# Kernel optimization log

Measured on AMD Instinct MI355X. Metric: run time of the kernel, lower is better.

Reference implementation:

```python
import jax, jax.numpy as jnp
import numpy as np

N_NODES = 100000
N_EDGES = 3200000
IN_F, HID, OUT = 24, 64, 1


def _gcn_conv(x, W, b, src, dst, norm, n):
    # x: [N, Fin] -> h: [N, Fout]; PyG GCNConv: lin first, then normalized aggregation, then bias
    h = x @ W                                    # [N, Fout]
    msg = h[src] * norm[:, None]                 # [E+N, Fout] gathered, norm-weighted messages
    agg = jax.ops.segment_sum(msg, dst, num_segments=n)  # scatter-add to targets
    return agg + b


def setup_inputs() -> dict:
    key = jax.random.key(0)
    k1, k2, k3, k4 = jax.random.split(key, 4)
    x = jax.random.normal(k1, (N_NODES, IN_F), dtype=jnp.float32)
    edge_index = jax.random.randint(k2, (2, N_EDGES), 0, N_NODES, dtype=jnp.int64)
    # Glorot-ish init for weights
    W1 = jax.random.normal(k3, (IN_F, HID), dtype=jnp.float32) / np.sqrt(IN_F)
    b1 = jnp.zeros((HID,), dtype=jnp.float32)
    W2 = jax.random.normal(k4, (HID, OUT), dtype=jnp.float32) / np.sqrt(HID)
    b2 = jnp.zeros((OUT,), dtype=jnp.float32)
    return {"x": x, "edge_index": edge_index, "W1": W1, "b1": b1, "W2": W2, "b2": b2}


def reference(x, edge_index, W1, b1, W2, b2):
    n = x.shape[0]
    # add self-loops (PyG GCNConv default)
    loops = jnp.arange(n, dtype=edge_index.dtype)
    src = jnp.concatenate([edge_index[0], loops])
    dst = jnp.concatenate([edge_index[1], loops])
    # symmetric normalization: deg over targets of A+I, norm_e = d^-1/2[src] * d^-1/2[dst]
    deg = jax.ops.segment_sum(jnp.ones_like(dst, dtype=x.dtype), dst, num_segments=n)
    dinv = jnp.where(deg > 0, jax.lax.rsqrt(deg), 0.0)
    norm = dinv[src] * dinv[dst]
    h = _gcn_conv(x, W1, b1, src, dst, norm, n)
    h = jax.nn.relu(h)
    # F.dropout with training=self.training -> identity in eval mode (reference runs eval)
    out = _gcn_conv(h, W2, b2, src, dst, norm, n)
    return out
```

## Files before the change

### kernel.cpp

```cpp
#include <hip/hip_runtime.h>
#include <hip/hip_fp16.h>

#define IN_F 24
#define HID 64
#define NB 512
#define NPB 256
#define GSZ_MAX 256
#define PBUF 7168
#define SRC_BITS 17

typedef unsigned int u32;

__device__ __forceinline__ int bucket_lo(int b, int n) {
    return (int)(((long long)b * n + NB - 1) / NB);
}

__global__ __launch_bounds__(256) void k_pcount(const int* __restrict__ dst,
                                                u32* __restrict__ pc, int e, int n) {
    __shared__ u32 h[NB];
    for (int j = threadIdx.x; j < NB; j += 256) h[j] = 0;
    __syncthreads();
    int blk = blockIdx.x;
    long long begin = (long long)e * blk / NPB;
    long long end   = (long long)e * (blk + 1) / NPB;
    for (long long i = begin + threadIdx.x; i < end; i += 256) {
        int k = (int)((long long)dst[i] * NB / n);
        atomicAdd(&h[k], 1u);
    }
    __syncthreads();
    for (int j = threadIdx.x; j < NB; j += 256) pc[(size_t)blk * NB + j] = h[j];
}

__global__ __launch_bounds__(256) void k_pscan_a(u32* __restrict__ pc,
                                                 u32* __restrict__ colsum) {
    __shared__ u32 ps[256];
    int t = blockIdx.x;
    int tid = threadIdx.x;
    u32 v = pc[(size_t)tid * NB + t];
    ps[tid] = v;
    __syncthreads();
    for (int off = 1; off < 256; off <<= 1) {
        u32 v2 = (tid >= off) ? ps[tid - off] : 0;
        __syncthreads();
        ps[tid] += v2;
        __syncthreads();
    }
    pc[(size_t)tid * NB + t] = ps[tid] - v;
    if (tid == 255) colsum[t] = ps[255];
}

__global__ void k_pscan_b(const u32* __restrict__ colsum, u32* __restrict__ basep) {
    __shared__ u32 s[NB];
    int t = threadIdx.x;
    u32 v = colsum[t];
    s[t] = v;
    __syncthreads();
    for (int off = 1; off < NB; off <<= 1) {
        u32 v2 = (t >= off) ? s[t - off] : 0;
        __syncthreads();
        s[t] += v2;
        __syncthreads();
    }
    basep[t] = s[t] - v;
}

__global__ __launch_bounds__(256) void k_part(const int* __restrict__ src,
                                              const int* __restrict__ dst,
                                              const u32* __restrict__ pc,
                                              const u32* __restrict__ basep,
                                              u32* __restrict__ pairs, int e, int n) {
    __shared__ u32 cur[NB];
    int blk = (blockIdx.x & 7) * (NPB / 8) + (blockIdx.x >> 3);
    for (int j = threadIdx.x; j < NB; j += 256)
        cur[j] = pc[(size_t)blk * NB + j] + basep[j];
    __syncthreads();
    long long begin = (long long)e * blk / NPB;
    long long end   = (long long)e * (blk + 1) / NPB;
    for (long long i = begin + threadIdx.x; i < end; i += 256) {
        int d = dst[i];
        int sv = src[i];
        int k = (int)((long long)d * NB / n);
        u32 loc = (u32)(d - bucket_lo(k, n));
        u32 pos = atomicAdd(&cur[k], 1u);
        pairs[pos] = (loc << SRC_BITS) | (u32)sv;
    }
}

__global__ __launch_bounds__(256) void k_bucket(const u32* __restrict__ pairs,
                                                const u32* __restrict__ basep,
                                                const float* __restrict__ x,
                                                int* __restrict__ cnt,
                                                int* __restrict__ row_start,
                                                float* __restrict__ dinv,
                                                int* __restrict__ csr_src,
                                                __half2* __restrict__ xs2, int e, int n) {
    __shared__ u32 pbuf[PBUF];
    __shared__ u32 h[GSZ_MAX];
    __shared__ u32 cur[GSZ_MAX];
    __shared__ u32 sc[GSZ_MAX];
    __shared__ float dloc[GSZ_MAX];
    int b = blockIdx.x;
    int lo = bucket_lo(b, n);
    int hi = bucket_lo(b + 1, n);
    int gsz = hi - lo;
    u32 start = basep[b];
    u32 endp = (b + 1 < NB) ? basep[b + 1] : (u32)e;
    int nbp = (int)(endp - start);
    for (int j = threadIdx.x; j < GSZ_MAX; j += 256) h[j] = 0;
    __syncthreads();
    int stored = nbp < PBUF ? nbp : PBUF;
    for (int i = threadIdx.x; i < stored; i += 256) {
        u32 p = pairs[start + i];
        pbuf[i] = p;
        atomicAdd(&h[p >> SRC_BITS], 1u);
    }
    for (int i = PBUF + threadIdx.x; i < nbp; i += 256) {
        atomicAdd(&h[pairs[start + i] >> SRC_BITS], 1u);
    }
    __syncthreads();
    int t = threadIdx.x;
    u32 v = h[t];
    sc[t] = v;
    __syncthreads();
    for (int off = 1; off < 256; off <<= 1) {
        u32 v2 = (t >= off) ? sc[t - off] : 0;
        __syncthreads();
        sc[t] += v2;
        __syncthreads();
    }
    u32 excl = sc[t] - v;
    if (t < gsz) {
        float dv = rsqrtf((float)(v + 1));
        cnt[lo + t] = (int)v;
        row_start[lo + t] = (int)(start + excl);
        dinv[lo + t] = dv;
        dloc[t] = dv;
        cur[t] = excl;
    }
    __syncthreads();
    for (int i = threadIdx.x; i < stored; i += 256) {
        u32 p = pbuf[i];
        u32 pos = atomicAdd(&cur[p >> SRC_BITS], 1u);
        csr_src[start + pos] = (int)(p & ((1u << SRC_BITS) - 1));
    }
    for (int i = PBUF + threadIdx.x; i < nbp; i += 256) {
        u32 p = pairs[start + i];
        u32 pos = atomicAdd(&cur[p >> SRC_BITS], 1u);
        csr_src[start + pos] = (int)(p & ((1u << SRC_BITS) - 1));
    }
    const float2* xf = (const float2*)(x + (long long)lo * IN_F);
    for (int i = threadIdx.x; i < gsz * 12; i += 256) {
        float2 vv = xf[i];
        float dn = dloc[i / 12];
        xs2[(long long)lo * 12 + i] = __floats2half2_rn(vv.x * dn, vv.y * dn);
    }
}

__global__ __launch_bounds__(256) void k_agg_hz(const float* __restrict__ x,
                                                const __half2* __restrict__ xs2,
                                                const float* __restrict__ dinv,
                                                const int* __restrict__ row_start,
                                                const int* __restrict__ cnt,
                                                const int* __restrict__ csr_src,
                                                const float* __restrict__ W1,
                                                const float* __restrict__ b1,
                                                const float* __restrict__ W2,
                                                float* __restrict__ zs, int n) {
    __shared__ float w[IN_F * HID];
    __shared__ float w2s[HID];
    __shared__ float b1s[HID];
    for (int j = threadIdx.x; j < IN_F * HID; j += 256) w[j] = W1[j];
    if (threadIdx.x < HID) { w2s[threadIdx.x] = W2[threadIdx.x]; b1s[threadIdx.x] = b1[threadIdx.x]; }
    __syncthreads();
    int g = threadIdx.x >> 3;
    int f4 = threadIdx.x & 7;
    int node = blockIdx.x * 32 + g;
    if (node >= n) return;
    float dn = dinv[node];
    const uint2* xq = (const uint2*)xs2;
    float ax0 = 0.0f, ay0 = 0.0f, ax1 = 0.0f, ay1 = 0.0f;
    if (f4 < 6) {
        int row = row_start[node];
        int c = cnt[node];
        float a0 = 0.0f, b0 = 0.0f, c0 = 0.0f, d0 = 0.0f;
        float a1 = 0.0f, b1v = 0.0f, c1 = 0.0f, d1 = 0.0f;
        int j = 0;
        for (; j + 16 <= c; j += 16) {
            const int* cp = csr_src + row + j;
            int s[16];
#pragma unroll
            for (int t = 0; t < 16; ++t) s[t] = cp[t];
            uint2 u[16];
#pragma unroll
            for (int t = 0; t < 16; ++t) u[t] = xq[(size_t)((u32)s[t] * 6u + (u32)f4)];
#pragma unroll
            for (int t = 0; t < 16; t += 2) {
                float2 e0 = __half22float2(__builtin_bit_cast(__half2, u[t].x));
                float2 e1 = __half22float2(__builtin_bit_cast(__half2, u[t].y));
                float2 o0 = __half22float2(__builtin_bit_cast(__half2, u[t + 1].x));
                float2 o1 = __half22float2(__builtin_bit_cast(__half2, u[t + 1].y));
                a0 += e0.x; b0 += e0.y; c0 += e1.x; d0 += e1.y;
                a1 += o0.x; b1v += o0.y; c1 += o1.x; d1 += o1.y;
            }
        }
        for (; j + 8 <= c; j += 8) {
            const int* cp = csr_src + row + j;
            int s[8];
#pragma unroll
            for (int t = 0; t < 8; ++t) s[t] = cp[t];
            uint2 u[8];
#pragma unroll
            for (int t = 0; t < 8; ++t) u[t] = xq[(size_t)((u32)s[t] * 6u + (u32)f4)];
#pragma unroll
            for (int t = 0; t < 8; t += 2) {
                float2 e0 = __half22float2(__builtin_bit_cast(__half2, u[t].x));
                float2 e1 = __half22float2(__builtin_bit_cast(__half2, u[t].y));
                float2 o0 = __half22float2(__builtin_bit_cast(__half2, u[t + 1].x));
                float2 o1 = __half22float2(__builtin_bit_cast(__half2, u[t + 1].y));
                a0 += e0.x; b0 += e0.y; c0 += e1.x; d0 += e1.y;
                a1 += o0.x; b1v += o0.y; c1 += o1.x; d1 += o1.y;
            }
        }
        for (; j < c; ++j) {
            int s = csr_src[row + j];
            uint2 u = xq[(size_t)((u32)s * 6u + (u32)f4)];
            float2 e0 = __half22float2(__builtin_bit_cast(__half2, u.x));
            float2 e1 = __half22float2(__builtin_bit_cast(__half2, u.y));
            a0 += e0.x; b0 += e0.y; c0 += e1.x; d0 += e1.y;
        }
        ax0 = a0 + a1; ay0 = b0 + b1v; ax1 = c0 + c1; ay1 = d0 + d1;
        float4 sx4 = *(const float4*)(x + (long long)node * IN_F + 4 * f4);
        ax0 = (ax0 + sx4.x * dn) * dn;
        ay0 = (ay0 + sx4.y * dn) * dn;
        ax1 = (ax1 + sx4.z * dn) * dn;
        ay1 = (ay1 + sx4.w * dn) * dn;
    }
    int fb = f4 * 8;
    float h[8];
#pragma unroll
    for (int jj = 0; jj < 8; ++jj) h[jj] = b1s[fb + jj];
#pragma unroll
    for (int k = 0; k < IN_F; ++k) {
        int sl = k >> 2;
        int r = k & 3;
        float xv;
        if (r == 0)      xv = __shfl(ax0, sl, 8);
        else if (r == 1) xv = __shfl(ay0, sl, 8);
        else if (r == 2) xv = __shfl(ax1, sl, 8);
        else             xv = __shfl(ay1, sl, 8);
        const float* wr = w + k * HID + fb;
#pragma unroll
        for (int jj = 0; jj < 8; ++jj) h[jj] += xv * wr[jj];
    }
    float p = 0.0f;
#pragma unroll
    for (int jj = 0; jj < 8; ++jj) p += fmaxf(h[jj], 0.0f) * w2s[fb + jj];
    p += __shfl_down(p, 4, 8);
    p += __shfl_down(p, 2, 8);
    p += __shfl_down(p, 1, 8);
    if (f4 == 0) zs[node] = p * dn;
}

__global__ void k_out(const float* __restrict__ zs, const float* __restrict__ dinv,
                      const int* __restrict__ row_start, const int* __restrict__ cnt,
                      const int* __restrict__ csr_src, const float* __restrict__ b2,
                      float* __restrict__ out, int n) {
    int t = blockIdx.x * blockDim.x + threadIdx.x;
    int node = t >> 4;
    int lane = t & 15;
    if (node >= n) return;
    int row = row_start[node];
    int c = cnt[node];
    float v = 0.0f;
    for (int j = lane; j < c; j += 16) {
        v += zs[csr_src[row + j]];
    }
    v += __shfl_down(v, 8, 16);
    v += __shfl_down(v, 4, 16);
    v += __shfl_down(v, 2, 16);
    v += __shfl_down(v, 1, 16);
    if (lane == 0) {
        out[node] = b2[0] + dinv[node] * (zs[node] + v);
    }
}

extern "C" void kernel_launch(void* const* d_in, const int* in_sizes, int n_in,
                              void* d_out, int out_size, void* d_ws, size_t ws_size,
                              hipStream_t stream) {
    const float* x   = (const float*)d_in[0];
    const int*   ei  = (const int*)d_in[1];
    const float* W1  = (const float*)d_in[2];
    const float* b1  = (const float*)d_in[3];
    const float* W2  = (const float*)d_in[4];
    const float* b2  = (const float*)d_in[5];
    float* out = (float*)d_out;

    const int n = in_sizes[0] / IN_F;
    const int e = in_sizes[1] / 2;
    const int* src = ei;
    const int* dst = ei + e;

    const int B = 256;

    char* base = (char*)d_ws;
    u32* pairs     = (u32*)base;
    float* zs      = (float*)base;
    size_t ov = ((size_t)e * 4 + 255) & ~(size_t)255;
    char* after    = base + ov;
    int* cnt       = (int*)after;
    int* row_start = cnt + n;
    int* csr_src   = row_start + n;
    float* dinv    = (float*)(csr_src + e);
    __half* xs     = (__half*)(dinv + n);
    u32* pc        = (u32*)(xs + (size_t)n * IN_F);
    u32* colsum    = pc + (size_t)NPB * NB;
    u32* basep     = colsum + NB;

    k_pcount<<<NPB, B, 0, stream>>>(dst, pc, e, n);
    k_pscan_a<<<NB, B, 0, stream>>>(pc, colsum);
    k_pscan_b<<<1, NB, 0, stream>>>(colsum, basep);
    k_part<<<NPB, B, 0, stream>>>(src, dst, pc, basep, pairs, e, n);
    k_bucket<<<NB, B, 0, stream>>>(pairs, basep, x, cnt, row_start, dinv, csr_src,
                                   (__half2*)xs, e, n);

    k_agg_hz<<<(n + 31) / 32, B, 0, stream>>>(x, (const __half2*)xs, dinv,
                                              row_start, cnt, csr_src,
                                              W1, b1, W2, zs, n);

    const long long n16 = (long long)n * 16;
    k_out<<<(int)((n16 + B - 1) / B), B, 0, stream>>>(zs, dinv, row_start, cnt, csr_src, b2, out, n);
}
```

Before: 218.1 us.

## Split feature gather into two half-width passes over separate fp16 tables

The fp16 scaled-feature table is stored as two separate 12-feature halves, and the layer-1 aggregation now runs as two kernels. Each kernel gathers only one half, so the random-access working set per pass is halved (2.4MB instead of 4.8MB) and more of it can stay in cache. The first pass writes partial aggregates to a workspace buffer, and the second reads them back before applying W1, ReLU and W2. The cost is a second traversal of the CSR indices, an extra intermediate write and read, and one more kernel launch.

```diff
diff --git a/kernel.cpp b/kernel.cpp
--- a/kernel.cpp
+++ b/kernel.cpp
@@ -151,17 +151,99 @@
     const float2* xf = (const float2*)(x + (long long)lo * IN_F);
     for (int i = threadIdx.x; i < gsz * 12; i += 256) {
         float2 vv = xf[i];
-        float dn = dloc[i / 12];
-        xs2[(long long)lo * 12 + i] = __floats2half2_rn(vv.x * dn, vv.y * dn);
-    }
-}
-
-__global__ __launch_bounds__(256) void k_agg_hz(const float* __restrict__ x,
-                                                const __half2* __restrict__ xs2,
+        int nd = i / 12;
+        int u = i - nd * 12;
+        float dn = dloc[nd];
+        __half2 hv = __floats2half2_rn(vv.x * dn, vv.y * dn);
+        long long rowbase = (long long)(lo + nd) * 6;
+        if (u < 6) xs2[rowbase + u] = hv;
+        else       xs2[(long long)n * 6 + rowbase + (u - 6)] = hv;
+    }
+}
+
+__device__ __forceinline__ void gather_acc(const uint2* __restrict__ xq,
+                                           const int* __restrict__ cp0, int c, int f4,
+                                           float& AX0, float& AY0, float& AX1, float& AY1) {
+    float a0 = 0.0f, b0 = 0.0f, c0 = 0.0f, d0 = 0.0f;
+    float a1 = 0.0f, b1v = 0.0f, c1 = 0.0f, d1 = 0.0f;
+    int j = 0;
+    for (; j + 16 <= c; j += 16) {
+        const int* cp = cp0 + j;
+        int s[16];
+#pragma unroll
+        for (int t = 0; t < 16; ++t) s[t] = cp[t];
+        uint2 u[16];
+#pragma unroll
+        for (int t = 0; t < 16; ++t) u[t] = xq[(size_t)((u32)s[t] * 3u + (u32)f4)];
+#pragma unroll
+        for (int t = 0; t < 16; t += 2) {
+            float2 e0 = __half22float2(__builtin_bit_cast(__half2, u[t].x));
+            float2 e1 = __half22float2(__builtin_bit_cast(__half2, u[t].y));
+            float2 o0 = __half22float2(__builtin_bit_cast(__half2, u[t + 1].x));
+            float2 o1 = __half22float2(__builtin_bit_cast(__half2, u[t + 1].y));
+            a0 += e0.x; b0 += e0.y; c0 += e1.x; d0 += e1.y;
+            a1 += o0.x; b1v += o0.y; c1 += o1.x; d1 += o1.y;
+        }
+    }
+    for (; j + 8 <= c; j += 8) {
+        const int* cp = cp0 + j;
+        int s[8];
+#pragma unroll
+        for (int t = 0; t < 8; ++t) s[t] = cp[t];
+        uint2 u[8];
+#pragma unroll
+        for (int t = 0; t < 8; ++t) u[t] = xq[(size_t)((u32)s[t] * 3u + (u32)f4)];
+#pragma unroll
+        for (int t = 0; t < 8; t += 2) {
+            float2 e0 = __half22float2(__builtin_bit_cast(__half2, u[t].x));
+            float2 e1 = __half22float2(__builtin_bit_cast(__half2, u[t].y));
+            float2 o0 = __half22float2(__builtin_bit_cast(__half2, u[t + 1].x));
+            float2 o1 = __half22float2(__builtin_bit_cast(__half2, u[t + 1].y));
+            a0 += e0.x; b0 += e0.y; c0 += e1.x; d0 += e1.y;
+            a1 += o0.x; b1v += o0.y; c1 += o1.x; d1 += o1.y;
+        }
+    }
+    for (; j < c; ++j) {
+        int s = cp0[j];
+        uint2 u = xq[(size_t)((u32)s * 3u + (u32)f4)];
+        float2 e0 = __half22float2(__builtin_bit_cast(__half2, u.x));
+        float2 e1 = __half22float2(__builtin_bit_cast(__half2, u.y));
+        a0 += e0.x; b0 += e0.y; c0 += e1.x; d0 += e1.y;
+    }
+    AX0 = a0 + a1; AY0 = b0 + b1v; AX1 = c0 + c1; AY1 = d0 + d1;
+}
+
+__global__ __launch_bounds__(256) void k_agg_p0(const uint2* __restrict__ xq0,
+                                                const float* __restrict__ x,
                                                 const float* __restrict__ dinv,
                                                 const int* __restrict__ row_start,
                                                 const int* __restrict__ cnt,
                                                 const int* __restrict__ csr_src,
+                                                float* __restrict__ a0, int n) {
+    int g = threadIdx.x >> 2;
+    int f4 = threadIdx.x & 3;
+    int node = blockIdx.x * 64 + g;
+    if (node >= n) return;
+    if (f4 >= 3) return;
+    float dn = dinv[node];
+    float ax0, ay0, ax1, ay1;
+    gather_acc(xq0, csr_src + row_start[node], cnt[node], f4, ax0, ay0, ax1, ay1);
+    float4 sx4 = *(const float4*)(x + (long long)node * IN_F + 4 * f4);
+    float4 r;
+    r.x = (ax0 + sx4.x * dn) * dn;
+    r.y = (ay0 + sx4.y * dn) * dn;
+    r.z = (ax1 + sx4.z * dn) * dn;
+    r.w = (ay1 + sx4.w * dn) * dn;
+    ((float4*)(a0 + (long long)node * 12))[f4] = r;
+}
+
+__global__ __launch_bounds__(256) void k_agg_p1(const uint2* __restrict__ xq1,
+                                                const float* __restrict__ x,
+                                                const float* __restrict__ dinv,
+                                                const int* __restrict__ row_start,
+                                                const int* __restrict__ cnt,
+                                                const int* __restrict__ csr_src,
+                                                const float* __restrict__ a0,
                                                 const float* __restrict__ W1,
                                                 const float* __restrict__ b1,
                                                 const float* __restrict__ W2,
@@ -172,92 +254,57 @@
     for (int j = threadIdx.x; j < IN_F * HID; j += 256) w[j] = W1[j];
     if (threadIdx.x < HID) { w2s[threadIdx.x] = W2[threadIdx.x]; b1s[threadIdx.x] = b1[threadIdx.x]; }
     __syncthreads();
-    int g = threadIdx.x >> 3;
-    int f4 = threadIdx.x & 7;
-    int node = blockIdx.x * 32 + g;
+    int g = threadIdx.x >> 2;
+    int f4 = threadIdx.x & 3;
+    int node = blockIdx.x * 64 + g;
     if (node >= n) return;
     float dn = dinv[node];
-    const uint2* xq = (const uint2*)xs2;
     float ax0 = 0.0f, ay0 = 0.0f, ax1 = 0.0f, ay1 = 0.0f;
-    if (f4 < 6) {
-        int row = row_start[node];
-        int c = cnt[node];
-        float a0 = 0.0f, b0 = 0.0f, c0 = 0.0f, d0 = 0.0f;
-        float a1 = 0.0f, b1v = 0.0f, c1 = 0.0f, d1 = 0.0f;
-        int j = 0;
-        for (; j + 16 <= c; j += 16) {
-            const int* cp = csr_src + row + j;
-            int s[16];
-#pragma unroll
-            for (int t = 0; t < 16; ++t) s[t] = cp[t];
-            uint2 u[16];
-#pragma unroll
-            for (int t = 0; t < 16; ++t) u[t] = xq[(size_t)((u32)s[t] * 6u + (u32)f4)];
-#pragma unroll
-            for (int t = 0; t < 16; t += 2) {
-                float2 e0 = __half22float2(__builtin_bit_cast(__half2, u[t].x));
-                float2 e1 = __half22float2(__builtin_bit_cast(__half2, u[t].y));
-                float2 o0 = __half22float2(__builtin_bit_cast(__half2, u[t + 1].x));
-                float2 o1 = __half22float2(__builtin_bit_cast(__half2, u[t + 1].y));
-                a0 += e0.x; b0 += e0.y; c0 += e1.x; d0 += e1.y;
-                a1 += o0.x; b1v += o0.y; c1 += o1.x; d1 += o1.y;
-            }
-        }
-        for (; j + 8 <= c; j += 8) {
-            const int* cp = csr_src + row + j;
-            int s[8];
-#pragma unroll
-            for (int t = 0; t < 8; ++t) s[t] = cp[t];
-            uint2 u[8];
-#pragma unroll
-            for (int t = 0; t < 8; ++t) u[t] = xq[(size_t)((u32)s[t] * 6u + (u32)f4)];
-#pragma unroll
-            for (int t = 0; t < 8; t += 2) {
-                float2 e0 = __half22float2(__builtin_bit_cast(__half2, u[t].x));
-                float2 e1 = __half22float2(__builtin_bit_cast(__half2, u[t].y));
-                float2 o0 = __half22float2(__builtin_bit_cast(__half2, u[t + 1].x));
-                float2 o1 = __half22float2(__builtin_bit_cast(__half2, u[t + 1].y));
-                a0 += e0.x; b0 += e0.y; c0 += e1.x; d0 += e1.y;
-                a1 += o0.x; b1v += o0.y; c1 += o1.x; d1 += o1.y;
-            }
-        }
-        for (; j < c; ++j) {
-            int s = csr_src[row + j];
-            uint2 u = xq[(size_t)((u32)s * 6u + (u32)f4)];
-            float2 e0 = __half22float2(__builtin_bit_cast(__half2, u.x));
-            float2 e1 = __half22float2(__builtin_bit_cast(__half2, u.y));
-            a0 += e0.x; b0 += e0.y; c0 += e1.x; d0 += e1.y;
-        }
-        ax0 = a0 + a1; ay0 = b0 + b1v; ax1 = c0 + c1; ay1 = d0 + d1;
-        float4 sx4 = *(const float4*)(x + (long long)node * IN_F + 4 * f4);
+    float4 old = make_float4(0.0f, 0.0f, 0.0f, 0.0f);
+    if (f4 < 3) {
+        gather_acc(xq1, csr_src + row_start[node], cnt[node], f4, ax0, ay0, ax1, ay1);
+        float4 sx4 = *(const float4*)(x + (long long)node * IN_F + 12 + 4 * f4);
         ax0 = (ax0 + sx4.x * dn) * dn;
         ay0 = (ay0 + sx4.y * dn) * dn;
         ax1 = (ax1 + sx4.z * dn) * dn;
         ay1 = (ay1 + sx4.w * dn) * dn;
-    }
-    int fb = f4 * 8;
-    float h[8];
-#pragma unroll
-    for (int jj = 0; jj < 8; ++jj) h[jj] = b1s[fb + jj];
-#pragma unroll
-    for (int k = 0; k < IN_F; ++k) {
+        old = ((const float4*)(a0 + (long long)node * 12))[f4];
+    }
+    int fb = f4 * 16;
+    float h[16];
+#pragma unroll
+    for (int jj = 0; jj < 16; ++jj) h[jj] = b1s[fb + jj];
+#pragma unroll
+    for (int k = 0; k < 12; ++k) {
         int sl = k >> 2;
         int r = k & 3;
         float xv;
-        if (r == 0)      xv = __shfl(ax0, sl, 8);
-        else if (r == 1) xv = __shfl(ay0, sl, 8);
-        else if (r == 2) xv = __shfl(ax1, sl, 8);
-        else             xv = __shfl(ay1, sl, 8);
+        if (r == 0)      xv = __shfl(old.x, sl, 4);
+        else if (r == 1) xv = __shfl(old.y, sl, 4);
+        else if (r == 2) xv = __shfl(old.z, sl, 4);
+        else             xv = __shfl(old.w, sl, 4);
         const float* wr = w + k * HID + fb;
 #pragma unroll
-        for (int jj = 0; jj < 8; ++jj) h[jj] += xv * wr[jj];
+        for (int jj = 0; jj < 16; ++jj) h[jj] += xv * wr[jj];
+    }
+#pragma unroll
+    for (int k = 0; k < 12; ++k) {
+        int sl = k >> 2;
+        int r = k & 3;
+        float xv;
+        if (r == 0)      xv = __shfl(ax0, sl, 4);
+        else if (r == 1) xv = __shfl(ay0, sl, 4);
+        else if (r == 2) xv = __shfl(ax1, sl, 4);
+        else             xv = __shfl(ay1, sl, 4);
+        const float* wr = w + (12 + k) * HID + fb;
+#pragma unroll
+        for (int jj = 0; jj < 16; ++jj) h[jj] += xv * wr[jj];
     }
     float p = 0.0f;
 #pragma unroll
-    for (int jj = 0; jj < 8; ++jj) p += fmaxf(h[jj], 0.0f) * w2s[fb + jj];
-    p += __shfl_down(p, 4, 8);
-    p += __shfl_down(p, 2, 8);
-    p += __shfl_down(p, 1, 8);
+    for (int jj = 0; jj < 16; ++jj) p += fmaxf(h[jj], 0.0f) * w2s[fb + jj];
+    p += __shfl_down(p, 2, 4);
+    p += __shfl_down(p, 1, 4);
     if (f4 == 0) zs[node] = p * dn;
 }
 
@@ -305,6 +352,8 @@
     char* base = (char*)d_ws;
     u32* pairs     = (u32*)base;
     float* zs      = (float*)base;
+    size_t zsb = ((size_t)n * 4 + 255) & ~(size_t)255;
+    float* a0      = (float*)(base + zsb);
     size_t ov = ((size_t)e * 4 + 255) & ~(size_t)255;
     char* after    = base + ov;
     int* cnt       = (int*)after;
@@ -316,6 +365,9 @@
     u32* colsum    = pc + (size_t)NPB * NB;
     u32* basep     = colsum + NB;
 
+    const uint2* xq0 = (const uint2*)xs;
+    const uint2* xq1 = (const uint2*)(xs + (size_t)n * 12);
+
     k_pcount<<<NPB, B, 0, stream>>>(dst, pc, e, n);
     k_pscan_a<<<NB, B, 0, stream>>>(pc, colsum);
     k_pscan_b<<<1, NB, 0, stream>>>(colsum, basep);
@@ -323,9 +375,10 @@
     k_bucket<<<NB, B, 0, stream>>>(pairs, basep, x, cnt, row_start, dinv, csr_src,
                                    (__half2*)xs, e, n);
 
-    k_agg_hz<<<(n + 31) / 32, B, 0, stream>>>(x, (const __half2*)xs, dinv,
-                                              row_start, cnt, csr_src,
-                                              W1, b1, W2, zs, n);
+    const int nblk = (n + 63) / 64;
+    k_agg_p0<<<nblk, B, 0, stream>>>(xq0, x, dinv, row_start, cnt, csr_src, a0, n);
+    k_agg_p1<<<nblk, B, 0, stream>>>(xq1, x, dinv, row_start, cnt, csr_src, a0,
+                                     W1, b1, W2, zs, n);
 
     const long long n16 = (long long)n * 16;
     k_out<<<(int)((n16 + B - 1) / B), B, 0, stream>>>(zs, dinv, row_start, cnt, csr_src, b2, out, n);
```

Measured after the change: 232.9 us. 1.07x slower.
